# Kernel optimization log

Measured on AMD Instinct MI355X. Metric: run time of the kernel, lower is better.

The kernel has to match this reference:

```python
import jax, jax.numpy as jnp
import numpy as np
import math

def setup_inputs() -> dict:
    key = jax.random.key(0)
    qkv = jax.random.normal(key, (64, 192, 2048), dtype=jnp.float32)
    return {"qkv": qkv}

def reference(qkv):
    # qkv: [N, 3C, T]
    ch = qkv.shape[1] // 3
    q, k, v = jnp.split(qkv, 3, axis=1)  # each [N, C, T]
    scale = 1.0 / math.sqrt(math.sqrt(ch))
    # scores: [N, T, S]
    weight = jnp.einsum('bct,bcs->bts', q * scale, k * scale)
    weight = jax.nn.softmax(weight.astype(jnp.float32), axis=-1).astype(qkv.dtype)
    return jnp.einsum('bts,bcs->bct', weight, v)  # [N, C, T]
```

## Files before the change

kernel.cpp:

```cpp
#include <hip/hip_runtime.h>
#include <hip/hip_bf16.h>

typedef __attribute__((ext_vector_type(16))) float    f32x16;
typedef __attribute__((ext_vector_type(8)))  short    s16x8;
typedef __attribute__((ext_vector_type(2)))  unsigned u32x2;

#define NB    64
#define CH    64
#define TS    2048
#define QBLK  128
#define KVB   64
#define NKV   (TS / KVB)
#define KT_OFF  (16u * 1024 * 1024)
#define V_OFF   (32u * 1024 * 1024)
#define BSTRIDE (TS * CH * 2)
#define QSCALE  0.18033688011112042f

__device__ __forceinline__ unsigned f2bf(float f) {
    unsigned u = __float_as_uint(f);
    return (u + 0x7fffu + ((u >> 16) & 1u)) >> 16;
}
__device__ __forceinline__ unsigned cvtpk(float lo, float hi) {
    unsigned r;
    asm("v_cvt_pk_bf16_f32 %0, %1, %2" : "=v"(r) : "v"(lo), "v"(hi));
    return r;
}
__device__ __forceinline__ u32x2 plswap(unsigned x, unsigned y) {
#if __has_builtin(__builtin_amdgcn_permlane32_swap)
    return __builtin_amdgcn_permlane32_swap(x, y, false, false);
#else
    asm("v_permlane32_swap_b32 %0, %1" : "+v"(x), "+v"(y));
    u32x2 r; r.x = x; r.y = y; return r;
#endif
}
__device__ __forceinline__ float crosshalf_sum(float x) {
    const u32x2 r = plswap(__float_as_uint(x), __float_as_uint(x));
    return __uint_as_float(r.x) + __uint_as_float(r.y);
}
__device__ __forceinline__ void gload16(const void* g, void* l) {
    __builtin_amdgcn_global_load_lds(
        (const __attribute__((address_space(1))) void*)g,
        (__attribute__((address_space(3))) void*)l, 16, 0, 0);
}

__global__ __launch_bounds__(256)
void prep_all(const float* __restrict__ qkv, char* __restrict__ ws)
{
    __shared__ float tile[64][65];
    const int bid = (int)blockIdx.x;
    if (bid < NB * 64) {
        const int b     = bid >> 6;
        const int rt    = bid & 63;
        const int which = rt >> 5;
        const int tt    = rt & 31;
        const float* src = qkv + ((size_t)b * 192 + which * 64) * TS + tt * 64;

        const int c  = threadIdx.x >> 2;
        const int tq = (threadIdx.x & 3) * 16;
        const float4* s4 = (const float4*)(src + (size_t)c * TS + tq);
        #pragma unroll
        for (int j = 0; j < 4; ++j) {
            const float4 f = s4[j];
            tile[c][tq + 4*j + 0] = f.x;
            tile[c][tq + 4*j + 1] = f.y;
            tile[c][tq + 4*j + 2] = f.z;
            tile[c][tq + 4*j + 3] = f.w;
        }
        __syncthreads();

        const int t  = threadIdx.x >> 2;
        const int cq = (threadIdx.x & 3) * 16;
        const float sc = which ? 1.0f : QSCALE;
        unsigned pk[8];
        #pragma unroll
        for (int j = 0; j < 8; ++j) {
            const float f0 = tile[cq + 2*j][t] * sc;
            const float f1 = tile[cq + 2*j + 1][t] * sc;
            pk[j] = f2bf(f0) | (f2bf(f1) << 16);
        }
        char* dst = ws + (which ? KT_OFF : 0u) +
                    (size_t)b * BSTRIDE + ((size_t)tt * 64 + t) * 128 + cq * 2;
        ((uint4*)dst)[0] = make_uint4(pk[0], pk[1], pk[2], pk[3]);
        ((uint4*)dst)[1] = make_uint4(pk[4], pk[5], pk[6], pk[7]);
    } else {
        const size_t e   = ((size_t)(bid - NB * 64) * 256 + threadIdx.x) * 16;
        const int b      = (int)(e >> 17);
        const size_t rem = e & 131071;
        const float4* src = (const float4*)(qkv + (size_t)b * 393216 + 262144 + rem);
        unsigned pk[8];
        #pragma unroll
        for (int j = 0; j < 4; ++j) {
            const float4 f = src[j];
            pk[2*j]     = f2bf(f.x) | (f2bf(f.y) << 16);
            pk[2*j + 1] = f2bf(f.z) | (f2bf(f.w) << 16);
        }
        char* dst = ws + V_OFF + e * 2;
        ((uint4*)dst)[0] = make_uint4(pk[0], pk[1], pk[2], pk[3]);
        ((uint4*)dst)[1] = make_uint4(pk[4], pk[5], pk[6], pk[7]);
    }
}

template<bool DIRA>
__device__ __forceinline__ void attn_main(
    const char* __restrict__ qtb, const char* __restrict__ ktb,
    const char* __restrict__ vtb, float* __restrict__ ob,
    char* k_sm0, char* k_sm1, char* v_sm0, char* v_sm1,
    int t0, int lane, int wv)
{
    const int col = lane & 31;
    const int hi  = lane >> 5;

    s16x8 qfrag[4];
    {
        const int t = t0 + wv * 32 + col;
        const char* qrow = qtb + (size_t)t * 128 + hi * 16;
        #pragma unroll
        for (int ks = 0; ks < 4; ++ks)
            qfrag[ks] = *(const s16x8*)(qrow + ks * 32);
    }

    const int lr = lane >> 3, lx = lane & 7;
    const int krow = wv * 16 + lr;
    const unsigned koff = krow * 128  + ((lx ^ (krow & 7)) << 4);
    const unsigned voff = krow * 4096 + ((lx ^ (krow & 7)) << 4);
    const char* ksrc = ktb + koff;
    const char* vsrc = vtb + voff;
    char* kd0 = k_sm0 + wv * 2048;
    char* vd0 = v_sm0 + wv * 2048;
    char* kd1 = k_sm1 + wv * 2048;
    char* vd1 = v_sm1 + wv * 2048;

    f32x16 zf;
    f32x16 oacc0, oacc1;
    #pragma unroll
    for (int i = 0; i < 16; ++i) { zf[i] = 0.f; oacc0[i] = 0.f; oacc1[i] = 0.f; }
    float l_run = 0.f;

    gload16(ksrc, kd0);           gload16(ksrc + 1024, kd0 + 1024);
    gload16(vsrc, vd0);           gload16(vsrc + 32768, vd0 + 1024);
    __syncthreads();

    int cur = 0;
    for (int kt = 0; kt < NKV; ++kt) {
        if (kt + 1 < NKV) {
            const char* kp = ksrc + (size_t)(kt + 1) * 8192;
            const char* vp = vsrc + (size_t)(kt + 1) * 128;
            char* kd = cur ? kd0 : kd1;
            char* vd = cur ? vd0 : vd1;
            gload16(kp, kd);          gload16(kp + 1024, kd + 1024);
            gload16(vp, vd);          gload16(vp + 32768, vd + 1024);
        }
        const char* kb = cur ? k_sm1 : k_sm0;
        const char* vb = cur ? v_sm1 : v_sm0;

        f32x16 sa0, sa1;
        __builtin_amdgcn_s_setprio(1);
        #pragma unroll
        for (int ks = 0; ks < 4; ++ks) {
            const int sw = 32 * ks + 16 * hi;
            const s16x8 kf0 = *(const s16x8*)(kb + col * 128        + (sw ^ ((col & 7) << 4)));
            const s16x8 kf1 = *(const s16x8*)(kb + (32 + col) * 128 + (sw ^ ((col & 7) << 4)));
            if (ks == 0) {
                sa0 = __builtin_amdgcn_mfma_f32_32x32x16_bf16(kf0, qfrag[0], zf, 0, 0, 0);
                sa1 = __builtin_amdgcn_mfma_f32_32x32x16_bf16(kf1, qfrag[0], zf, 0, 0, 0);
            } else {
                sa0 = __builtin_amdgcn_mfma_f32_32x32x16_bf16(kf0, qfrag[ks], sa0, 0, 0, 0);
                sa1 = __builtin_amdgcn_mfma_f32_32x32x16_bf16(kf1, qfrag[ks], sa1, 0, 0, 0);
            }
        }
        __builtin_amdgcn_s_setprio(0);

        float p0[16], p1[16];
        float s0 = 0.f, s1 = 0.f, s2 = 0.f, s3 = 0.f;
        #pragma unroll
        for (int r = 0; r < 16; r += 2) {
            p0[r]     = __builtin_amdgcn_exp2f(sa0[r]);
            p0[r + 1] = __builtin_amdgcn_exp2f(sa0[r + 1]);
            p1[r]     = __builtin_amdgcn_exp2f(sa1[r]);
            p1[r + 1] = __builtin_amdgcn_exp2f(sa1[r + 1]);
            s0 += p0[r]; s1 += p0[r + 1]; s2 += p1[r]; s3 += p1[r + 1];
        }
        l_run += (s0 + s1) + (s2 + s3);

        unsigned pq0[8], pq1[8];
        #pragma unroll
        for (int q = 0; q < 8; ++q) {
            pq0[q] = cvtpk(p0[2*q], p0[2*q + 1]);
            pq1[q] = cvtpk(p1[2*q], p1[2*q + 1]);
        }

        __builtin_amdgcn_s_setprio(1);
        #pragma unroll
        for (int ks = 0; ks < 4; ++ks) {
            const int base = (ks & 1) * 4;
            unsigned a0, a1, a2, a3;
            if (ks < 2) { a0 = pq0[base]; a1 = pq0[base+1]; a2 = pq0[base+2]; a3 = pq0[base+3]; }
            else        { a0 = pq1[base]; a1 = pq1[base+1]; a2 = pq1[base+2]; a3 = pq1[base+3]; }
            unsigned u0, u1, u2, u3;
            if (DIRA) {
                const u32x2 r02 = plswap(a0, a2), r13 = plswap(a1, a3);
                u0 = r02.x; u2 = r02.y; u1 = r13.x; u3 = r13.y;
            } else {
                const u32x2 r02 = plswap(a2, a0), r13 = plswap(a3, a1);
                u0 = r02.y; u2 = r02.x; u1 = r13.y; u3 = r13.x;
            }
            union { unsigned u[4]; s16x8 v; } pb;
            pb.u[0] = u0; pb.u[1] = u1; pb.u[2] = u2; pb.u[3] = u3;
            const int sw = 32 * ks + 16 * hi;
            const s16x8 vf0 = *(const s16x8*)(vb + col * 128        + (sw ^ ((col & 7) << 4)));
            const s16x8 vf1 = *(const s16x8*)(vb + (32 + col) * 128 + (sw ^ ((col & 7) << 4)));
            oacc0 = __builtin_amdgcn_mfma_f32_32x32x16_bf16(vf0, pb.v, oacc0, 0, 0, 0);
            oacc1 = __builtin_amdgcn_mfma_f32_32x32x16_bf16(vf1, pb.v, oacc1, 0, 0, 0);
        }
        __builtin_amdgcn_s_setprio(0);
        __syncthreads();
        cur ^= 1;
    }

    const float inv = 1.0f / crosshalf_sum(l_run);
    const int t = t0 + wv * 32 + col;
    #pragma unroll
    for (int r = 0; r < 16; ++r) {
        const int c = (r & 3) + 8 * (r >> 2) + 4 * hi;
        ob[(size_t)c * TS + t]        = oacc0[r] * inv;
        ob[(size_t)(c + 32) * TS + t] = oacc1[r] * inv;
    }
}

__global__ __launch_bounds__(256, 4)
void qkv_attn_kernel(const char* __restrict__ ws, float* __restrict__ out)
{
    __shared__ __align__(16) char k_sm[2][KVB * 128];
    __shared__ __align__(16) char v_sm[2][CH * 128];

    const int tid  = threadIdx.x;
    const int lane = tid & 63;
    const int wv   = tid >> 6;

    const u32x2 pr = plswap((unsigned)lane, 100u + (unsigned)lane);
    const bool dirA = (__builtin_amdgcn_readfirstlane((int)pr.x) == 0);

    const int Dd      = (int)blockIdx.x;
    const int logical = (Dd & 7) * 128 + (Dd >> 3);
    const int b  = logical >> 4;
    const int qt = logical & 15;
    const int t0 = qt * QBLK;

    const char* qtb = ws + (size_t)b * BSTRIDE;
    const char* ktb = ws + KT_OFF + (size_t)b * BSTRIDE;
    const char* vtb = ws + V_OFF  + (size_t)b * BSTRIDE;
    float* ob       = out + (size_t)b * CH * TS;

    if (dirA)
        attn_main<true >(qtb, ktb, vtb, ob, k_sm[0], k_sm[1], v_sm[0], v_sm[1], t0, lane, wv);
    else
        attn_main<false>(qtb, ktb, vtb, ob, k_sm[0], k_sm[1], v_sm[0], v_sm[1], t0, lane, wv);
}

extern "C" void kernel_launch(void* const* d_in, const int* in_sizes, int n_in,
                              void* d_out, int out_size, void* d_ws, size_t ws_size,
                              hipStream_t stream) {
    const float* qkv = (const float*)d_in[0];
    float* outp      = (float*)d_out;
    char* ws         = (char*)d_ws;
    prep_all<<<dim3(NB * 64 + 2048), dim3(256), 0, stream>>>(qkv, ws);
    qkv_attn_kernel<<<dim3(NB * (TS / QBLK)), dim3(256), 0, stream>>>(ws, outp);
}
```

Before: 108.2 us.

## Process two query sub-tiles per wave, halving waves per block

Each wave now handles 64 query rows as two 32-row sub-tiles (A and B), reusing the K and V fragments it reads from LDS for both. The block shrinks to 128 threads (2 waves) and each thread issues four K/V async loads per tile instead of two. The A and B phases are interleaved so one sub-tile's exp/convert work can overlap the other's MFMAs. The aim is to cut LDS reads per MFMA and amortise barriers, at the cost of roughly twice the accumulator and fragment registers per wave, lower occupancy, and fewer waves to hide load latency.

```diff
diff --git a/kernel.cpp b/kernel.cpp
--- a/kernel.cpp
+++ b/kernel.cpp
@@ -105,39 +105,40 @@
     const char* __restrict__ qtb, const char* __restrict__ ktb,
     const char* __restrict__ vtb, float* __restrict__ ob,
     char* k_sm0, char* k_sm1, char* v_sm0, char* v_sm1,
-    int t0, int lane, int wv)
+    int t0, int tid)
 {
-    const int col = lane & 31;
-    const int hi  = lane >> 5;
-
-    s16x8 qfrag[4];
+    const int lane = tid & 63;
+    const int wv   = tid >> 6;
+    const int col  = lane & 31;
+    const int hi   = lane >> 5;
+
+    s16x8 qfA[4], qfB[4];
     {
-        const int t = t0 + wv * 32 + col;
-        const char* qrow = qtb + (size_t)t * 128 + hi * 16;
-        #pragma unroll
-        for (int ks = 0; ks < 4; ++ks)
-            qfrag[ks] = *(const s16x8*)(qrow + ks * 32);
-    }
-
-    const int lr = lane >> 3, lx = lane & 7;
-    const int krow = wv * 16 + lr;
-    const unsigned koff = krow * 128  + ((lx ^ (krow & 7)) << 4);
-    const unsigned voff = krow * 4096 + ((lx ^ (krow & 7)) << 4);
-    const char* ksrc = ktb + koff;
-    const char* vsrc = vtb + voff;
-    char* kd0 = k_sm0 + wv * 2048;
-    char* vd0 = v_sm0 + wv * 2048;
-    char* kd1 = k_sm1 + wv * 2048;
-    char* vd1 = v_sm1 + wv * 2048;
-
-    f32x16 zf;
-    f32x16 oacc0, oacc1;
+        const int tA = t0 + wv * 64 + col;
+        const char* qrowA = qtb + (size_t)tA * 128 + hi * 16;
+        #pragma unroll
+        for (int ks = 0; ks < 4; ++ks) {
+            qfA[ks] = *(const s16x8*)(qrowA + ks * 32);
+            qfB[ks] = *(const s16x8*)(qrowA + 32 * 128 + ks * 32);
+        }
+    }
+
+    const int rowbase = tid >> 3;
+    const int offX = (((tid & 7) ^ (rowbase & 7)) << 4);
+    const char* ksrc = ktb + rowbase * 128  + offX;
+    const char* vsrc = vtb + rowbase * 4096 + offX;
+    const int dst0 = tid * 16;
+
+    f32x16 zf, oA0, oA1, oB0, oB1;
     #pragma unroll
-    for (int i = 0; i < 16; ++i) { zf[i] = 0.f; oacc0[i] = 0.f; oacc1[i] = 0.f; }
-    float l_run = 0.f;
-
-    gload16(ksrc, kd0);           gload16(ksrc + 1024, kd0 + 1024);
-    gload16(vsrc, vd0);           gload16(vsrc + 32768, vd0 + 1024);
+    for (int i = 0; i < 16; ++i) { zf[i]=0.f; oA0[i]=0.f; oA1[i]=0.f; oB0[i]=0.f; oB1[i]=0.f; }
+    float lA = 0.f, lB = 0.f;
+
+    #pragma unroll
+    for (int c = 0; c < 4; ++c) {
+        gload16(ksrc + c * 2048,  k_sm0 + c * 2048 + dst0);
+        gload16(vsrc + c * 65536, v_sm0 + c * 2048 + dst0);
+    }
     __syncthreads();
 
     int cur = 0;
@@ -145,48 +146,85 @@
         if (kt + 1 < NKV) {
             const char* kp = ksrc + (size_t)(kt + 1) * 8192;
             const char* vp = vsrc + (size_t)(kt + 1) * 128;
-            char* kd = cur ? kd0 : kd1;
-            char* vd = cur ? vd0 : vd1;
-            gload16(kp, kd);          gload16(kp + 1024, kd + 1024);
-            gload16(vp, vd);          gload16(vp + 32768, vd + 1024);
+            char* kd = (cur ? k_sm0 : k_sm1) + dst0;
+            char* vd = (cur ? v_sm0 : v_sm1) + dst0;
+            #pragma unroll
+            for (int c = 0; c < 4; ++c) {
+                gload16(kp + c * 2048,  kd + c * 2048);
+                gload16(vp + c * 65536, vd + c * 2048);
+            }
         }
         const char* kb = cur ? k_sm1 : k_sm0;
         const char* vb = cur ? v_sm1 : v_sm0;
 
-        f32x16 sa0, sa1;
+        s16x8 kf0[4], kf1[4];
+        #pragma unroll
+        for (int ks = 0; ks < 4; ++ks) {
+            const int sw = 32 * ks + 16 * hi;
+            kf0[ks] = *(const s16x8*)(kb + col * 128        + (sw ^ ((col & 7) << 4)));
+            kf1[ks] = *(const s16x8*)(kb + (32 + col) * 128 + (sw ^ ((col & 7) << 4)));
+        }
+
+        f32x16 saA0, saA1;
         __builtin_amdgcn_s_setprio(1);
+        saA0 = __builtin_amdgcn_mfma_f32_32x32x16_bf16(kf0[0], qfA[0], zf, 0, 0, 0);
+        saA1 = __builtin_amdgcn_mfma_f32_32x32x16_bf16(kf1[0], qfA[0], zf, 0, 0, 0);
+        #pragma unroll
+        for (int ks = 1; ks < 4; ++ks) {
+            saA0 = __builtin_amdgcn_mfma_f32_32x32x16_bf16(kf0[ks], qfA[ks], saA0, 0, 0, 0);
+            saA1 = __builtin_amdgcn_mfma_f32_32x32x16_bf16(kf1[ks], qfA[ks], saA1, 0, 0, 0);
+        }
+        __builtin_amdgcn_s_setprio(0);
+
+        unsigned pqA0[8], pqA1[8];
+        {
+            float s0=0.f, s1=0.f, s2=0.f, s3=0.f;
+            #pragma unroll
+            for (int q = 0; q < 8; ++q) {
+                const float e0 = __builtin_amdgcn_exp2f(saA0[2*q]);
+                const float e1 = __builtin_amdgcn_exp2f(saA0[2*q+1]);
+                const float f0 = __builtin_amdgcn_exp2f(saA1[2*q]);
+                const float f1 = __builtin_amdgcn_exp2f(saA1[2*q+1]);
+                s0 += e0; s1 += e1; s2 += f0; s3 += f1;
+                pqA0[q] = cvtpk(e0, e1);
+                pqA1[q] = cvtpk(f0, f1);
+            }
+            lA += (s0 + s1) + (s2 + s3);
+        }
+
+        f32x16 saB0, saB1;
+        __builtin_amdgcn_s_setprio(1);
+        saB0 = __builtin_amdgcn_mfma_f32_32x32x16_bf16(kf0[0], qfB[0], zf, 0, 0, 0);
+        saB1 = __builtin_amdgcn_mfma_f32_32x32x16_bf16(kf1[0], qfB[0], zf, 0, 0, 0);
+        #pragma unroll
+        for (int ks = 1; ks < 4; ++ks) {
+            saB0 = __builtin_amdgcn_mfma_f32_32x32x16_bf16(kf0[ks], qfB[ks], saB0, 0, 0, 0);
+            saB1 = __builtin_amdgcn_mfma_f32_32x32x16_bf16(kf1[ks], qfB[ks], saB1, 0, 0, 0);
+        }
+        __builtin_amdgcn_s_setprio(0);
+
+        s16x8 vf0[4], vf1[4];
         #pragma unroll
         for (int ks = 0; ks < 4; ++ks) {
             const int sw = 32 * ks + 16 * hi;
-            const s16x8 kf0 = *(const s16x8*)(kb + col * 128        + (sw ^ ((col & 7) << 4)));
-            const s16x8 kf1 = *(const s16x8*)(kb + (32 + col) * 128 + (sw ^ ((col & 7) << 4)));
-            if (ks == 0) {
-                sa0 = __builtin_amdgcn_mfma_f32_32x32x16_bf16(kf0, qfrag[0], zf, 0, 0, 0);
-                sa1 = __builtin_amdgcn_mfma_f32_32x32x16_bf16(kf1, qfrag[0], zf, 0, 0, 0);
-            } else {
-                sa0 = __builtin_amdgcn_mfma_f32_32x32x16_bf16(kf0, qfrag[ks], sa0, 0, 0, 0);
-                sa1 = __builtin_amdgcn_mfma_f32_32x32x16_bf16(kf1, qfrag[ks], sa1, 0, 0, 0);
-            }
-        }
-        __builtin_amdgcn_s_setprio(0);
-
-        float p0[16], p1[16];
-        float s0 = 0.f, s1 = 0.f, s2 = 0.f, s3 = 0.f;
-        #pragma unroll
-        for (int r = 0; r < 16; r += 2) {
-            p0[r]     = __builtin_amdgcn_exp2f(sa0[r]);
-            p0[r + 1] = __builtin_amdgcn_exp2f(sa0[r + 1]);
-            p1[r]     = __builtin_amdgcn_exp2f(sa1[r]);
-            p1[r + 1] = __builtin_amdgcn_exp2f(sa1[r + 1]);
-            s0 += p0[r]; s1 += p0[r + 1]; s2 += p1[r]; s3 += p1[r + 1];
-        }
-        l_run += (s0 + s1) + (s2 + s3);
-
-        unsigned pq0[8], pq1[8];
-        #pragma unroll
-        for (int q = 0; q < 8; ++q) {
-            pq0[q] = cvtpk(p0[2*q], p0[2*q + 1]);
-            pq1[q] = cvtpk(p1[2*q], p1[2*q + 1]);
+            vf0[ks] = *(const s16x8*)(vb + col * 128        + (sw ^ ((col & 7) << 4)));
+            vf1[ks] = *(const s16x8*)(vb + (32 + col) * 128 + (sw ^ ((col & 7) << 4)));
+        }
+
+        unsigned pqB0[8], pqB1[8];
+        {
+            float s0=0.f, s1=0.f, s2=0.f, s3=0.f;
+            #pragma unroll
+            for (int q = 0; q < 8; ++q) {
+                const float e0 = __builtin_amdgcn_exp2f(saB0[2*q]);
+                const float e1 = __builtin_amdgcn_exp2f(saB0[2*q+1]);
+                const float f0 = __builtin_amdgcn_exp2f(saB1[2*q]);
+                const float f1 = __builtin_amdgcn_exp2f(saB1[2*q+1]);
+                s0 += e0; s1 += e1; s2 += f0; s3 += f1;
+                pqB0[q] = cvtpk(e0, e1);
+                pqB1[q] = cvtpk(f0, f1);
+            }
+            lB += (s0 + s1) + (s2 + s3);
         }
 
         __builtin_amdgcn_s_setprio(1);
@@ -194,8 +232,8 @@
         for (int ks = 0; ks < 4; ++ks) {
             const int base = (ks & 1) * 4;
             unsigned a0, a1, a2, a3;
-            if (ks < 2) { a0 = pq0[base]; a1 = pq0[base+1]; a2 = pq0[base+2]; a3 = pq0[base+3]; }
-            else        { a0 = pq1[base]; a1 = pq1[base+1]; a2 = pq1[base+2]; a3 = pq1[base+3]; }
+            if (ks < 2) { a0 = pqA0[base]; a1 = pqA0[base+1]; a2 = pqA0[base+2]; a3 = pqA0[base+3]; }
+            else        { a0 = pqA1[base]; a1 = pqA1[base+1]; a2 = pqA1[base+2]; a3 = pqA1[base+3]; }
             unsigned u0, u1, u2, u3;
             if (DIRA) {
                 const u32x2 r02 = plswap(a0, a2), r13 = plswap(a1, a3);
@@ -206,28 +244,47 @@
             }
             union { unsigned u[4]; s16x8 v; } pb;
             pb.u[0] = u0; pb.u[1] = u1; pb.u[2] = u2; pb.u[3] = u3;
-            const int sw = 32 * ks + 16 * hi;
-            const s16x8 vf0 = *(const s16x8*)(vb + col * 128        + (sw ^ ((col & 7) << 4)));
-            const s16x8 vf1 = *(const s16x8*)(vb + (32 + col) * 128 + (sw ^ ((col & 7) << 4)));
-            oacc0 = __builtin_amdgcn_mfma_f32_32x32x16_bf16(vf0, pb.v, oacc0, 0, 0, 0);
-            oacc1 = __builtin_amdgcn_mfma_f32_32x32x16_bf16(vf1, pb.v, oacc1, 0, 0, 0);
+            oA0 = __builtin_amdgcn_mfma_f32_32x32x16_bf16(vf0[ks], pb.v, oA0, 0, 0, 0);
+            oA1 = __builtin_amdgcn_mfma_f32_32x32x16_bf16(vf1[ks], pb.v, oA1, 0, 0, 0);
+        }
+        #pragma unroll
+        for (int ks = 0; ks < 4; ++ks) {
+            const int base = (ks & 1) * 4;
+            unsigned a0, a1, a2, a3;
+            if (ks < 2) { a0 = pqB0[base]; a1 = pqB0[base+1]; a2 = pqB0[base+2]; a3 = pqB0[base+3]; }
+            else        { a0 = pqB1[base]; a1 = pqB1[base+1]; a2 = pqB1[base+2]; a3 = pqB1[base+3]; }
+            unsigned u0, u1, u2, u3;
+            if (DIRA) {
+                const u32x2 r02 = plswap(a0, a2), r13 = plswap(a1, a3);
+                u0 = r02.x; u2 = r02.y; u1 = r13.x; u3 = r13.y;
+            } else {
+                const u32x2 r02 = plswap(a2, a0), r13 = plswap(a3, a1);
+                u0 = r02.y; u2 = r02.x; u1 = r13.y; u3 = r13.x;
+            }
+            union { unsigned u[4]; s16x8 v; } pb;
+            pb.u[0] = u0; pb.u[1] = u1; pb.u[2] = u2; pb.u[3] = u3;
+            oB0 = __builtin_amdgcn_mfma_f32_32x32x16_bf16(vf0[ks], pb.v, oB0, 0, 0, 0);
+            oB1 = __builtin_amdgcn_mfma_f32_32x32x16_bf16(vf1[ks], pb.v, oB1, 0, 0, 0);
         }
         __builtin_amdgcn_s_setprio(0);
         __syncthreads();
         cur ^= 1;
     }
 
-    const float inv = 1.0f / crosshalf_sum(l_run);
-    const int t = t0 + wv * 32 + col;
+    const float invA = 1.0f / crosshalf_sum(lA);
+    const float invB = 1.0f / crosshalf_sum(lB);
+    const int tA = t0 + wv * 64 + col;
     #pragma unroll
     for (int r = 0; r < 16; ++r) {
         const int c = (r & 3) + 8 * (r >> 2) + 4 * hi;
-        ob[(size_t)c * TS + t]        = oacc0[r] * inv;
-        ob[(size_t)(c + 32) * TS + t] = oacc1[r] * inv;
-    }
-}
-
-__global__ __launch_bounds__(256, 4)
+        ob[(size_t)c * TS + tA]             = oA0[r] * invA;
+        ob[(size_t)(c + 32) * TS + tA]      = oA1[r] * invA;
+        ob[(size_t)c * TS + tA + 32]        = oB0[r] * invB;
+        ob[(size_t)(c + 32) * TS + tA + 32] = oB1[r] * invB;
+    }
+}
+
+__global__ __launch_bounds__(128, 2)
 void qkv_attn_kernel(const char* __restrict__ ws, float* __restrict__ out)
 {
     __shared__ __align__(16) char k_sm[2][KVB * 128];
@@ -235,7 +292,6 @@
 
     const int tid  = threadIdx.x;
     const int lane = tid & 63;
-    const int wv   = tid >> 6;
 
     const u32x2 pr = plswap((unsigned)lane, 100u + (unsigned)lane);
     const bool dirA = (__builtin_amdgcn_readfirstlane((int)pr.x) == 0);
@@ -252,9 +308,9 @@
     float* ob       = out + (size_t)b * CH * TS;
 
     if (dirA)
-        attn_main<true >(qtb, ktb, vtb, ob, k_sm[0], k_sm[1], v_sm[0], v_sm[1], t0, lane, wv);
+        attn_main<true >(qtb, ktb, vtb, ob, k_sm[0], k_sm[1], v_sm[0], v_sm[1], t0, tid);
     else
-        attn_main<false>(qtb, ktb, vtb, ob, k_sm[0], k_sm[1], v_sm[0], v_sm[1], t0, lane, wv);
+        attn_main<false>(qtb, ktb, vtb, ob, k_sm[0], k_sm[1], v_sm[0], v_sm[1], t0, tid);
 }
 
 extern "C" void kernel_launch(void* const* d_in, const int* in_sizes, int n_in,
@@ -264,5 +320,5 @@
     float* outp      = (float*)d_out;
     char* ws         = (char*)d_ws;
     prep_all<<<dim3(NB * 64 + 2048), dim3(256), 0, stream>>>(qkv, ws);
-    qkv_attn_kernel<<<dim3(NB * (TS / QBLK)), dim3(256), 0, stream>>>(ws, outp);
-}
+    qkv_attn_kernel<<<dim3(NB * (TS / QBLK)), dim3(128), 0, stream>>>(ws, outp);
+}
```

Result: slower. 113.6 us (+5.0%).
